# Performance work log

Hardware: AMD Instinct MI355X
Metric: run time of the kernel (lower is better)

Reference implementation:

```python
import jax, jax.numpy as jnp
import numpy as np

B, L, D, H, S = 4, 4096, 1024, 16, 4
DH = D // H


def setup_inputs() -> dict:
    key = jax.random.key(0)
    ks = jax.random.split(key, 12)
    std = 0.02
    inp = {
        "x": jax.random.normal(ks[0], (B, L, D), jnp.float32),
        "scale_logits": jax.random.normal(ks[1], (S,), jnp.float32),
        "wq": jax.random.normal(ks[2], (D, D), jnp.float32) * std,
        "bq": jnp.zeros((D,), jnp.float32),
        "wk": jax.random.normal(ks[3], (D, D), jnp.float32) * std,
        "bk": jnp.zeros((D,), jnp.float32),
        "wv": jax.random.normal(ks[4], (D, D), jnp.float32) * std,
        "bv": jnp.zeros((D,), jnp.float32),
        "wo": jax.random.normal(ks[5], (D, D), jnp.float32) * std,
        "bo": jnp.zeros((D,), jnp.float32),
        "ws": jax.random.normal(ks[6], (S, D, D), jnp.float32) * std,  # per-scale Linear weights (out,in)
        "bs": jax.random.normal(ks[7], (S, D), jnp.float32) * std,
    }
    return inp


def reference(x, scale_logits, wq, bq, wk, bk, wv, bv, wo, bo, ws, bs):
    # q/k/v projections; kept flat (B,L,D) since the torch code re-flattens before scale proj
    qf = x @ wq.T + bq
    kf = x @ wk.T + bk
    vf = x @ wv.T + bv
    # per-scale linear projection, vectorized over scales: (B,S,L,D)
    sq = jnp.einsum('bld,sed->bsle', qf, ws) + bs[None, :, None, :]
    sk = jnp.einsum('bld,sed->bsle', kf, ws) + bs[None, :, None, :]
    sv = jnp.einsum('bld,sed->bsle', vf, ws) + bs[None, :, None, :]
    sq = sq.reshape(B, S, L, H, DH)
    sk = sk.reshape(B, S, L, H, DH)
    sv = sv.reshape(B, S, L, H, DH)
    # faithful to torch: matmul over last two dims of (B,L,H,dh) -> per-position
    # head-mixing scores of shape (B,S,L,H,H)
    scale = 1.0 / np.sqrt(DH).astype(np.float32)
    scores = jnp.einsum('bslhd,bslgd->bslhg', sq, sk) * scale
    attn = jax.nn.softmax(scores, axis=-1)
    out = jnp.einsum('bslhg,bslgd->bslhd', attn, sv)  # (B,S,L,H,DH)
    w = jax.nn.softmax(scale_logits, axis=0)  # (S,)
    combined = jnp.einsum('s,bslhd->blhd', w, out).reshape(B, L, D)
    return combined @ wo.T + bo
```

## Files before the change

kernel.cpp:

```cpp
#include <hip/hip_runtime.h>


typedef unsigned short u16;
typedef __attribute__((ext_vector_type(8))) short s16x8;
typedef __attribute__((ext_vector_type(8))) unsigned short u16x8;
typedef __attribute__((ext_vector_type(4))) float f32x4;

#define MM 16384
#define DDIM 1024
#define DDSQ 1048576ull

__device__ __forceinline__ u16 f2bf(float f) {
  unsigned u = __float_as_uint(f);
  u = (u + 0x7FFFu + ((u >> 16) & 1u)) >> 16;
  return (u16)u;
}
__device__ __forceinline__ float b2f(u16 b) {
  return __uint_as_float(((unsigned)b) << 16);
}
__device__ __forceinline__ void gload_lds16(const void* g, void* l) {
  __builtin_amdgcn_global_load_lds(
      (const __attribute__((address_space(1))) void*)g,
      (__attribute__((address_space(3))) void*)l, 16, 0, 0);
}

__global__ __launch_bounds__(256) void k_f32_to_bf16(
    const float* __restrict__ in, u16* __restrict__ out, int n4) {
  int i = blockIdx.x * 256 + threadIdx.x;
  if (i >= n4) return;
  float4 v = reinterpret_cast<const float4*>(in)[i];
  ushort4 o;
  o.x = f2bf(v.x); o.y = f2bf(v.y); o.z = f2bf(v.z); o.w = f2bf(v.w);
  reinterpret_cast<ushort4*>(out)[i] = o;
}

__global__ __launch_bounds__(256) void k_transpose_bf16(
    const float* __restrict__ wq, const float* __restrict__ wk,
    const float* __restrict__ wv, u16* __restrict__ out) {
  __shared__ float tile[32][33];
  const float* src = (blockIdx.z == 0) ? wq : (blockIdx.z == 1) ? wk : wv;
  u16* dst = out + (size_t)blockIdx.z * DDSQ;
  int tx = threadIdx.x, ty = threadIdx.y;
  int bx = blockIdx.x * 32, by = blockIdx.y * 32;
#pragma unroll
  for (int i = 0; i < 4; ++i)
    tile[ty + 8 * i][tx] = src[(size_t)(by + ty + 8 * i) * DDIM + bx + tx];
  __syncthreads();
#pragma unroll
  for (int i = 0; i < 4; ++i)
    dst[(size_t)(bx + ty + 8 * i) * DDIM + by + tx] = f2bf(tile[tx][ty + 8 * i]);
}

__global__ __launch_bounds__(256) void k_bias_fuse(
    const float* __restrict__ ws, const float* __restrict__ bq,
    const float* __restrict__ bk, const float* __restrict__ bv,
    const float* __restrict__ bs, float* __restrict__ bf) {
  int idx = blockIdx.y;
  int s = idx / 3, t = idx - s * 3;
  const float* bt = (t == 0) ? bq : (t == 1) ? bk : bv;
  int lane = threadIdx.x & 63, wid = threadIdx.x >> 6;
  int e = blockIdx.x * 4 + wid;
  const float* wr = ws + (size_t)s * DDSQ + (size_t)e * DDIM;
  float p = 0.f;
  for (int j = lane; j < DDIM; j += 64) p += wr[j] * bt[j];
#pragma unroll
  for (int off = 32; off > 0; off >>= 1) p += __shfl_xor(p, off);
  if (lane == 0) bf[idx * DDIM + e] = p + bs[s * DDIM + e];
}

template <typename OutT>
__global__ __launch_bounds__(512, 1) void k_gemm256(
    const u16* __restrict__ A, const u16* __restrict__ B, OutT* __restrict__ C,
    const float* __restrict__ bias, int M, int N, int K,
    size_t za, size_t zb, size_t zc, size_t zbias, int nbx, int zmode) {
  __shared__ u16 lds[4][2][8192];

  int z = blockIdx.x / nbx;
  int nb = blockIdx.x - z * nbx;
  const u16* Ag; const u16* Bg;
  if (zmode == 1) { Ag = A + (size_t)(z / 3) * za; Bg = B + (size_t)(z % 3) * zb; }
  else            { Ag = A + (size_t)z * za;       Bg = B + (size_t)z * zb; }
  OutT* Cg = C + (size_t)z * zc;
  const float* biasz = bias ? (bias + (size_t)z * zbias) : nullptr;

  int m0 = blockIdx.y * 256, n0 = nb * 256;
  int tid = threadIdx.x;
  int lane = tid & 63, wid = tid >> 6;
  int wm = wid >> 2, wn = wid & 3;
  int NT = K >> 5;

  int scb = ((lane & 3) * 16) ^ (((lane >> 3) & 3) << 4);
  const char* srcA[2]; const char* srcB[2]; int ldsc[2];
#pragma unroll
  for (int r = 0; r < 2; ++r) {
    int c = r * 8 + wid;
    int row = c * 16 + (lane >> 2);
    srcA[r] = (const char*)Ag + ((size_t)(m0 + row) * K) * 2 + scb;
    srcB[r] = (const char*)Bg + ((size_t)(n0 + row) * K) * 2 + scb;
    ldsc[r] = c * 1024;
  }
  char* lbase = (char*)&lds[0][0][0];

  int fxor = ((lane >> 4) * 16) ^ (((lane >> 1) & 3) << 4);
  int aoff = (wm * 128 + (lane & 15)) * 64 + fxor;
  int boff = (wn * 64 + (lane & 15)) * 64 + fxor;

  f32x4 acc[8][4] = {};
  s16x8 cA0[4], cA1[4], cB[4];
  s16x8 nA0[4], nA1[4], nB[4];

#define STAGE_A(kt, rg)                                                   \
  {                                                                       \
    _Pragma("unroll") for (int r = 0; r < 2; ++r)                         \
        gload_lds16(srcA[r] + (size_t)(kt) * 64,                          \
                    lbase + (rg) * 32768 + ldsc[r]);                      \
  }
#define STAGE_B(kt, rg)                                                   \
  {                                                                       \
    _Pragma("unroll") for (int r = 0; r < 2; ++r)                         \
        gload_lds16(srcB[r] + (size_t)(kt) * 64,                          \
                    lbase + (rg) * 32768 + 16384 + ldsc[r]);              \
  }

#define SUBITER(C0, C1, CBv, N0, N1, NBv, tcur)                           \
  {                                                                       \
    asm volatile("s_waitcnt vmcnt(4)" ::: "memory");                      \
    asm volatile("s_barrier" ::: "memory");                               \
    int tn = (tcur) + 1 < NT ? (tcur) + 1 : NT - 1;                       \
    const char* bA = lbase + (tn & 3) * 32768;                            \
    const char* bB = bA + 16384;                                          \
    _Pragma("unroll") for (int i = 0; i < 4; ++i)                         \
        NBv[i] = *(const s16x8*)(bB + boff + i * 1024);                   \
    _Pragma("unroll") for (int i = 0; i < 4; ++i)                         \
        N0[i] = *(const s16x8*)(bA + aoff + i * 1024);                    \
    _Pragma("unroll") for (int i = 0; i < 4; ++i)                         \
        N1[i] = *(const s16x8*)(bA + aoff + 4096 + i * 1024);             \
    int ts = (tcur) + 3 < NT ? (tcur) + 3 : NT - 1;                       \
    int rgs = ((tcur) + 3) & 3;                                           \
    STAGE_A(ts, rgs); STAGE_B(ts, rgs);                                   \
    _Pragma("unroll") for (int mi = 0; mi < 4; ++mi)                      \
      _Pragma("unroll") for (int ni = 0; ni < 4; ++ni)                    \
          acc[mi][ni] = __builtin_amdgcn_mfma_f32_16x16x32_bf16(          \
              C0[mi], CBv[ni], acc[mi][ni], 0, 0, 0);                     \
    _Pragma("unroll") for (int mi = 0; mi < 4; ++mi)                      \
      _Pragma("unroll") for (int ni = 0; ni < 4; ++ni)                    \
          acc[mi + 4][ni] = __builtin_amdgcn_mfma_f32_16x16x32_bf16(      \
              C1[mi], CBv[ni], acc[mi + 4][ni], 0, 0, 0);                 \
    _Pragma("unroll") for (int g = 0; g < 4; ++g) {                       \
      __builtin_amdgcn_sched_group_barrier(0x100, 3, 0);     \
      __builtin_amdgcn_sched_group_barrier(0x010, 1, 0);     \
      __builtin_amdgcn_sched_group_barrier(0x008, 8, 0);     \
    }                                                                     \
  }

  STAGE_A(0, 0); STAGE_B(0, 0);
  STAGE_A(1, 1); STAGE_B(1, 1);
  STAGE_A(2, 2); STAGE_B(2, 2);
  asm volatile("s_waitcnt vmcnt(8)" ::: "memory");
  asm volatile("s_barrier" ::: "memory");
  {
    const char* bA = lbase;
    const char* bB = bA + 16384;
#pragma unroll
    for (int i = 0; i < 4; ++i) cB[i]  = *(const s16x8*)(bB + boff + i * 1024);
#pragma unroll
    for (int i = 0; i < 4; ++i) cA0[i] = *(const s16x8*)(bA + aoff + i * 1024);
#pragma unroll
    for (int i = 0; i < 4; ++i)
      cA1[i] = *(const s16x8*)(bA + aoff + 4096 + i * 1024);
  }

  for (int t = 0; t < NT; t += 2) {
    SUBITER(cA0, cA1, cB, nA0, nA1, nB, t);
    SUBITER(nA0, nA1, nB, cA0, cA1, cB, t + 1);
  }
#undef SUBITER
#undef STAGE_A
#undef STAGE_B

  asm volatile("s_waitcnt vmcnt(0)" ::: "memory");

#pragma unroll
  for (int mi = 0; mi < 8; ++mi) {
#pragma unroll
    for (int ni = 0; ni < 4; ++ni) {
      int colg = n0 + wn * 64 + ni * 16 + (lane & 15);
      float badd = biasz ? biasz[colg] : 0.f;
#pragma unroll
      for (int r = 0; r < 4; ++r) {
        int rowg = m0 + wm * 128 + mi * 16 + ((lane >> 4) << 2) + r;
        float v = acc[mi][ni][r] + badd;
        if constexpr (sizeof(OutT) == 2) Cg[(size_t)rowg * N + colg] = f2bf(v);
        else                             Cg[(size_t)rowg * N + colg] = v;
      }
    }
  }
}

__global__ __launch_bounds__(256) void k_attn_all(
    const u16* __restrict__ proj, u16* __restrict__ outbf,
    const float* __restrict__ sl, int rows) {
  __shared__ u16 kv[4][2][1024];
  int lane = threadIdx.x & 63, wid = threadIdx.x >> 6;
  int row = blockIdx.x * 4 + wid;
  int h = lane >> 2, dq = lane & 3;
  int doff = h * 64 + dq * 16;

  float l0 = sl[0], l1 = sl[1], l2 = sl[2], l3 = sl[3];
  float lm = fmaxf(fmaxf(l0, l1), fmaxf(l2, l3));
  float e0 = __expf(l0 - lm), e1 = __expf(l1 - lm), e2 = __expf(l2 - lm),
        e3 = __expf(l3 - lm);
  float esum = e0 + e1 + e2 + e3;
  float wsc4[4] = {e0 / esum, e1 / esum, e2 / esum, e3 / esum};

  float acc[16];
#pragma unroll
  for (int i = 0; i < 16; ++i) acc[i] = 0.f;

  for (int s = 0; s < 4; ++s) {
    const u16* kr = proj + ((size_t)(3 * s + 1) * rows + row) * DDIM;
    const u16* vr = proj + ((size_t)(3 * s + 2) * rows + row) * DDIM;
    asm volatile("s_waitcnt vmcnt(0) lgkmcnt(0)" ::: "memory");
    gload_lds16(kr + lane * 8,       &kv[wid][0][0]);
    gload_lds16(kr + 512 + lane * 8, &kv[wid][0][512]);
    gload_lds16(vr + lane * 8,       &kv[wid][1][0]);
    gload_lds16(vr + 512 + lane * 8, &kv[wid][1][512]);

    const u16* qr = proj + ((size_t)(3 * s) * rows + row) * DDIM + doff;
    u16x8 q0 = *reinterpret_cast<const u16x8*>(qr);
    u16x8 q1 = *reinterpret_cast<const u16x8*>(qr + 8);
    float qf[16];
#pragma unroll
    for (int i = 0; i < 8; ++i) {
      qf[i]     = b2f(q0[i]) * 0.125f;
      qf[8 + i] = b2f(q1[i]) * 0.125f;
    }
    asm volatile("s_waitcnt vmcnt(0)" ::: "memory");

    float sc[16];
#pragma unroll
    for (int g = 0; g < 16; ++g) {
      const u16* kp = &kv[wid][0][g * 64 + dq * 16];
      u16x8 k0 = *reinterpret_cast<const u16x8*>(kp);
      u16x8 k1 = *reinterpret_cast<const u16x8*>(kp + 8);
      float d = 0.f;
#pragma unroll
      for (int i = 0; i < 8; ++i) d = fmaf(qf[i], b2f(k0[i]), d);
#pragma unroll
      for (int i = 0; i < 8; ++i) d = fmaf(qf[8 + i], b2f(k1[i]), d);
      d += __shfl_xor(d, 1);
      d += __shfl_xor(d, 2);
      sc[g] = d;
    }

    float mx = sc[0];
#pragma unroll
    for (int g = 1; g < 16; ++g) mx = fmaxf(mx, sc[g]);
    float sum = 0.f;
#pragma unroll
    for (int g = 0; g < 16; ++g) { sc[g] = __expf(sc[g] - mx); sum += sc[g]; }
    float inv = wsc4[s] / sum;
#pragma unroll
    for (int g = 0; g < 16; ++g) sc[g] *= inv;

#pragma unroll
    for (int g = 0; g < 16; ++g) {
      float a = sc[g];
      const u16* vp = &kv[wid][1][g * 64 + dq * 16];
      u16x8 v0 = *reinterpret_cast<const u16x8*>(vp);
      u16x8 v1 = *reinterpret_cast<const u16x8*>(vp + 8);
#pragma unroll
      for (int i = 0; i < 8; ++i) {
        acc[i]     = fmaf(a, b2f(v0[i]), acc[i]);
        acc[8 + i] = fmaf(a, b2f(v1[i]), acc[8 + i]);
      }
    }
  }

  u16* op = outbf + (size_t)row * DDIM + doff;
  u16x8 o0, o1;
#pragma unroll
  for (int i = 0; i < 8; ++i) {
    o0[i] = f2bf(acc[i]);
    o1[i] = f2bf(acc[8 + i]);
  }
  *reinterpret_cast<u16x8*>(op) = o0;
  *reinterpret_cast<u16x8*>(op + 8) = o1;
}

extern "C" void kernel_launch(void* const* d_in, const int* in_sizes, int n_in,
                              void* d_out, int out_size, void* d_ws,
                              size_t ws_size, hipStream_t stream) {
  const float* x  = (const float*)d_in[0];
  const float* sl = (const float*)d_in[1];
  const float* wq = (const float*)d_in[2];
  const float* bq = (const float*)d_in[3];
  const float* wk = (const float*)d_in[4];
  const float* bk = (const float*)d_in[5];
  const float* wv = (const float*)d_in[6];
  const float* bv = (const float*)d_in[7];
  const float* wo = (const float*)d_in[8];
  const float* bo = (const float*)d_in[9];
  const float* ws = (const float*)d_in[10];
  const float* bs = (const float*)d_in[11];
  float* out = (float*)d_out;

  char* wsb = (char*)d_ws;
  size_t off = 0;
  u16* xbf    = (u16*)(wsb + off); off += (size_t)MM * DDIM * 2;
  u16* wfus   = (u16*)(wsb + off); off += 12ull * DDSQ * 2;
  u16* wobf   = (u16*)(wsb + off); off += DDSQ * 2;
  float* bfus = (float*)(wsb + off); off += 65536;
  u16* combc  = (u16*)(wsb + off); off += (size_t)MM * DDIM * 2;
  char* dynr  = wsb + off;
  size_t fixed = off;

  int chunk = 4096;
  while (chunk > 1024 && fixed + (size_t)12 * chunk * DDIM * 2 > ws_size)
    chunk >>= 1;
  u16* projc = (u16*)dynr;
  u16* wtT  = (u16*)dynr;
  u16* wsbf = (u16*)(dynr + 3ull * DDSQ * 2);

  int n4;
  n4 = MM * DDIM / 4;
  k_f32_to_bf16<<<(n4 + 255) / 256, 256, 0, stream>>>(x, xbf, n4);
  n4 = (int)(4 * DDSQ / 4);
  k_f32_to_bf16<<<(n4 + 255) / 256, 256, 0, stream>>>(ws, wsbf, n4);
  n4 = (int)(DDSQ / 4);
  k_f32_to_bf16<<<(n4 + 255) / 256, 256, 0, stream>>>(wo, wobf, n4);

  k_transpose_bf16<<<dim3(32, 32, 3), dim3(32, 8), 0, stream>>>(wq, wk, wv, wtT);
  k_bias_fuse<<<dim3(256, 12), 256, 0, stream>>>(ws, bq, bk, bv, bs, bfus);

  k_gemm256<u16><<<dim3(48, 4), 512, 0, stream>>>(
      wsbf, wtT, wfus, nullptr, 1024, 1024, 1024, DDSQ, DDSQ, DDSQ, 0, 4, 1);

  int nchunks = MM / chunk;
  for (int c = 0; c < nchunks; ++c) {
    const u16* xa = xbf + (size_t)c * chunk * DDIM;
    k_gemm256<u16><<<dim3(48, chunk / 256), 512, 0, stream>>>(
        xa, wfus, projc, bfus, chunk, 1024, 1024,
        0, DDSQ, (size_t)chunk * DDIM, DDIM, 4, 0);
    k_attn_all<<<dim3(chunk / 4), 256, 0, stream>>>(
        projc, combc + (size_t)c * chunk * DDIM, sl, chunk);
  }

  k_gemm256<float><<<dim3(4, 64), 512, 0, stream>>>(
      combc, wobf, out, bo, MM, 1024, 1024, 0, 0, 0, 0, 4, 0);
}
```

Baseline: 741.0 us.

## Double-buffer attention K/V loads, merge conversions, use setprio in GEMM

The attention kernel now double-buffers the per-scale K/V rows in LDS, prefetching the next scale while computing the current one, which hides global load latency. The three f32-to-bf16 conversion launches are merged into one grid-stride kernel, saving launch overhead. In the GEMM inner loop the sched_group_barrier interleaving hints are replaced with s_setprio around the MFMA block. That removal may change the instruction schedule in either direction, and double buffering doubles the LDS used per block.

```diff
diff --git a/kernel.cpp b/kernel.cpp
--- a/kernel.cpp
+++ b/kernel.cpp
@@ -24,14 +24,22 @@
       (__attribute__((address_space(3))) void*)l, 16, 0, 0);
 }
 
-__global__ __launch_bounds__(256) void k_f32_to_bf16(
-    const float* __restrict__ in, u16* __restrict__ out, int n4) {
-  int i = blockIdx.x * 256 + threadIdx.x;
-  if (i >= n4) return;
-  float4 v = reinterpret_cast<const float4*>(in)[i];
-  ushort4 o;
-  o.x = f2bf(v.x); o.y = f2bf(v.y); o.z = f2bf(v.z); o.w = f2bf(v.w);
-  reinterpret_cast<ushort4*>(out)[i] = o;
+__global__ __launch_bounds__(256) void k_cvt3(
+    const float* __restrict__ a, u16* __restrict__ oa, int na,
+    const float* __restrict__ b, u16* __restrict__ ob, int nb,
+    const float* __restrict__ c, u16* __restrict__ oc, int nc) {
+  int total = na + nb + nc;
+  for (int i = blockIdx.x * 256 + threadIdx.x; i < total;
+       i += gridDim.x * 256) {
+    const float* src; u16* dst; int j = i;
+    if (j < na)            { src = a; dst = oa; }
+    else if ((j -= na) < nb) { src = b; dst = ob; }
+    else                   { j -= nb; src = c; dst = oc; }
+    float4 v = reinterpret_cast<const float4*>(src)[j];
+    ushort4 o;
+    o.x = f2bf(v.x); o.y = f2bf(v.y); o.z = f2bf(v.z); o.w = f2bf(v.w);
+    reinterpret_cast<ushort4*>(dst)[j] = o;
+  }
 }
 
 __global__ __launch_bounds__(256) void k_transpose_bf16(
@@ -121,7 +129,6 @@
         gload_lds16(srcB[r] + (size_t)(kt) * 64,                          \
                     lbase + (rg) * 32768 + 16384 + ldsc[r]);              \
   }
-
 #define SUBITER(C0, C1, CBv, N0, N1, NBv, tcur)                           \
   {                                                                       \
     asm volatile("s_waitcnt vmcnt(4)" ::: "memory");                      \
@@ -138,6 +145,7 @@
     int ts = (tcur) + 3 < NT ? (tcur) + 3 : NT - 1;                       \
     int rgs = ((tcur) + 3) & 3;                                           \
     STAGE_A(ts, rgs); STAGE_B(ts, rgs);                                   \
+    __builtin_amdgcn_s_setprio(1);                                        \
     _Pragma("unroll") for (int mi = 0; mi < 4; ++mi)                      \
       _Pragma("unroll") for (int ni = 0; ni < 4; ++ni)                    \
           acc[mi][ni] = __builtin_amdgcn_mfma_f32_16x16x32_bf16(          \
@@ -146,11 +154,7 @@
       _Pragma("unroll") for (int ni = 0; ni < 4; ++ni)                    \
           acc[mi + 4][ni] = __builtin_amdgcn_mfma_f32_16x16x32_bf16(      \
               C1[mi], CBv[ni], acc[mi + 4][ni], 0, 0, 0);                 \
-    _Pragma("unroll") for (int g = 0; g < 4; ++g) {                       \
-      __builtin_amdgcn_sched_group_barrier(0x100, 3, 0);     \
-      __builtin_amdgcn_sched_group_barrier(0x010, 1, 0);     \
-      __builtin_amdgcn_sched_group_barrier(0x008, 8, 0);     \
-    }                                                                     \
+    __builtin_amdgcn_s_setprio(0);                                        \
   }
 
   STAGE_A(0, 0); STAGE_B(0, 0);
@@ -200,7 +204,7 @@
 __global__ __launch_bounds__(256) void k_attn_all(
     const u16* __restrict__ proj, u16* __restrict__ outbf,
     const float* __restrict__ sl, int rows) {
-  __shared__ u16 kv[4][2][1024];
+  __shared__ u16 kv[4][2][2][1024];
   int lane = threadIdx.x & 63, wid = threadIdx.x >> 6;
   int row = blockIdx.x * 4 + wid;
   int h = lane >> 2, dq = lane & 3;
@@ -213,34 +217,45 @@
   float esum = e0 + e1 + e2 + e3;
   float wsc4[4] = {e0 / esum, e1 / esum, e2 / esum, e3 / esum};
 
+#define KV_ISSUE(s, buf)                                                   \
+  {                                                                        \
+    const u16* kr = proj + ((size_t)(3 * (s) + 1) * rows + row) * DDIM;    \
+    const u16* vr = proj + ((size_t)(3 * (s) + 2) * rows + row) * DDIM;    \
+    gload_lds16(kr + lane * 8,       &kv[wid][buf][0][0]);                 \
+    gload_lds16(kr + 512 + lane * 8, &kv[wid][buf][0][512]);               \
+    gload_lds16(vr + lane * 8,       &kv[wid][buf][1][0]);                 \
+    gload_lds16(vr + 512 + lane * 8, &kv[wid][buf][1][512]);               \
+  }
+
+  KV_ISSUE(0, 0);
+
   float acc[16];
 #pragma unroll
   for (int i = 0; i < 16; ++i) acc[i] = 0.f;
 
   for (int s = 0; s < 4; ++s) {
-    const u16* kr = proj + ((size_t)(3 * s + 1) * rows + row) * DDIM;
-    const u16* vr = proj + ((size_t)(3 * s + 2) * rows + row) * DDIM;
-    asm volatile("s_waitcnt vmcnt(0) lgkmcnt(0)" ::: "memory");
-    gload_lds16(kr + lane * 8,       &kv[wid][0][0]);
-    gload_lds16(kr + 512 + lane * 8, &kv[wid][0][512]);
-    gload_lds16(vr + lane * 8,       &kv[wid][1][0]);
-    gload_lds16(vr + 512 + lane * 8, &kv[wid][1][512]);
+    int buf = s & 1;
 
     const u16* qr = proj + ((size_t)(3 * s) * rows + row) * DDIM + doff;
     u16x8 q0 = *reinterpret_cast<const u16x8*>(qr);
     u16x8 q1 = *reinterpret_cast<const u16x8*>(qr + 8);
+
+    if (s < 3) KV_ISSUE(s + 1, buf ^ 1);
+
+    if (s < 3) asm volatile("s_waitcnt vmcnt(6)" ::: "memory");
+    else       asm volatile("s_waitcnt vmcnt(0)" ::: "memory");
+
     float qf[16];
 #pragma unroll
     for (int i = 0; i < 8; ++i) {
       qf[i]     = b2f(q0[i]) * 0.125f;
       qf[8 + i] = b2f(q1[i]) * 0.125f;
     }
-    asm volatile("s_waitcnt vmcnt(0)" ::: "memory");
 
     float sc[16];
 #pragma unroll
     for (int g = 0; g < 16; ++g) {
-      const u16* kp = &kv[wid][0][g * 64 + dq * 16];
+      const u16* kp = &kv[wid][buf][0][g * 64 + dq * 16];
       u16x8 k0 = *reinterpret_cast<const u16x8*>(kp);
       u16x8 k1 = *reinterpret_cast<const u16x8*>(kp + 8);
       float d = 0.f;
@@ -266,7 +281,7 @@
 #pragma unroll
     for (int g = 0; g < 16; ++g) {
       float a = sc[g];
-      const u16* vp = &kv[wid][1][g * 64 + dq * 16];
+      const u16* vp = &kv[wid][buf][1][g * 64 + dq * 16];
       u16x8 v0 = *reinterpret_cast<const u16x8*>(vp);
       u16x8 v1 = *reinterpret_cast<const u16x8*>(vp + 8);
 #pragma unroll
@@ -276,6 +291,7 @@
       }
     }
   }
+#undef KV_ISSUE
 
   u16* op = outbf + (size_t)row * DDIM + doff;
   u16x8 o0, o1;
@@ -322,13 +338,10 @@
   u16* wtT  = (u16*)dynr;
   u16* wsbf = (u16*)(dynr + 3ull * DDSQ * 2);
 
-  int n4;
-  n4 = MM * DDIM / 4;
-  k_f32_to_bf16<<<(n4 + 255) / 256, 256, 0, stream>>>(x, xbf, n4);
-  n4 = (int)(4 * DDSQ / 4);
-  k_f32_to_bf16<<<(n4 + 255) / 256, 256, 0, stream>>>(ws, wsbf, n4);
-  n4 = (int)(DDSQ / 4);
-  k_f32_to_bf16<<<(n4 + 255) / 256, 256, 0, stream>>>(wo, wobf, n4);
+  k_cvt3<<<2048, 256, 0, stream>>>(
+      x, xbf, MM * DDIM / 4,
+      ws, wsbf, (int)(4 * DDSQ / 4),
+      wo, wobf, (int)(DDSQ / 4));
 
   k_transpose_bf16<<<dim3(32, 32, 3), dim3(32, 8), 0, stream>>>(wq, wk, wv, wtT);
   k_bias_fuse<<<dim3(256, 12), 256, 0, stream>>>(ws, bq, bk, bv, bs, bfus);
```

After: 715.5 us. 3.4% less time.
